# Kernel optimization log

Measured on AMD Instinct MI355X. Metric: run time of the kernel, lower is better.

Reference implementation:

```python
import jax, jax.numpy as jnp
import numpy as np

B, F, Q, CHUNK = 2, 8192, 4096, 512
NUM_VERTS = 6000


def _safe_div(n, d):
    return n / jnp.where(d == 0, 1.0, d)


def _bary(a, b, c, p):
    """Barycentric coords of the closest point on triangle (a,b,c) to p.
    All args broadcastable [..., 3]; returns [..., 3] (u, v, w) with
    closest = u*a + v*b + w*c. Ericson, Real-Time Collision Detection."""
    ab = b - a; ac = c - a; ap = p - a
    d1 = jnp.sum(ab * ap, -1); d2 = jnp.sum(ac * ap, -1)
    bp = p - b
    d3 = jnp.sum(ab * bp, -1); d4 = jnp.sum(ac * bp, -1)
    cp_ = p - c
    d5 = jnp.sum(ab * cp_, -1); d6 = jnp.sum(ac * cp_, -1)
    vc = d1 * d4 - d3 * d2
    vb = d5 * d2 - d1 * d6
    va = d3 * d6 - d5 * d4
    v_ab = _safe_div(d1, d1 - d3)
    w_ac = _safe_div(d2, d2 - d6)
    w_bc = _safe_div(d4 - d3, (d4 - d3) + (d5 - d6))
    inv = _safe_div(1.0, va + vb + vc)
    v_in = vb * inv; w_in = vc * inv
    zero = jnp.zeros_like(d1); one = jnp.ones_like(d1)
    conds = [(d1 <= 0) & (d2 <= 0),
             (d3 >= 0) & (d4 <= d3),
             (vc <= 0) & (d1 >= 0) & (d3 <= 0),
             (d6 >= 0) & (d5 <= d6),
             (vb <= 0) & (d2 >= 0) & (d6 <= 0),
             (va <= 0) & (d4 >= d3) & (d5 >= d6)]
    u = jnp.select(conds, [one, zero, 1 - v_ab, zero, 1 - w_ac, zero], 1 - v_in - w_in)
    v = jnp.select(conds, [zero, one, v_ab, zero, zero, 1 - w_bc], v_in)
    w = jnp.select(conds, [zero, zero, zero, one, w_ac, w_bc], w_in)
    return jnp.stack([u, v, w], -1)


def _closest_faces(triangles, points, chunk=CHUNK):
    """Exact closest-triangle index per query point (replaces BVH search).
    triangles [B,F,3,3], points [B,Q,3] -> int32 [B,Q]."""
    tri = jax.lax.stop_gradient(triangles)
    pts = jax.lax.stop_gradient(points)
    bsz, nq = pts.shape[0], pts.shape[1]
    a = tri[:, :, 0]; b = tri[:, :, 1]; c = tri[:, :, 2]  # [B,F,3]

    def one_chunk(p_chunk):  # [B,CH,3]
        pa = p_chunk[:, :, None, :]                       # [B,CH,1,3]
        bc = _bary(a[:, None], b[:, None], c[:, None], pa)  # [B,CH,F,3]
        cp = (bc[..., 0:1] * a[:, None] + bc[..., 1:2] * b[:, None]
              + bc[..., 2:3] * c[:, None])                # [B,CH,F,3]
        d2 = jnp.sum((cp - pa) ** 2, -1)                  # [B,CH,F]
        return jnp.argmin(d2, axis=-1)                    # [B,CH]

    chunks = jnp.moveaxis(pts.reshape(bsz, nq // chunk, chunk, 3), 1, 0)
    idx = jax.lax.map(one_chunk, chunks)                  # [NC,B,CH]
    return jnp.moveaxis(idx, 0, 1).reshape(bsz, nq)


def setup_inputs() -> dict:
    key = jax.random.key(0)
    k1, k2, k3, k4, k5 = jax.random.split(key, 5)
    return {
        'triangles': jax.random.normal(k1, (B, F, 3, 3), dtype=jnp.float32),
        'points': jax.random.normal(k2, (B, Q, 3), dtype=jnp.float32),
        'normals': jax.random.normal(k3, (B, F, 3, 3), dtype=jnp.float32),
        'cmaps': jax.random.normal(k4, (B, F, 3, 3), dtype=jnp.float32),
        'faces': jax.random.randint(k5, (B, F, 3), 0, NUM_VERTS, dtype=jnp.int32),
    }


def reference(triangles, points, normals, cmaps, faces):
    closest_faces = _closest_faces(triangles, points)     # [B,Q]
    idx = closest_faces[:, :, None, None]
    tri_g = jnp.take_along_axis(triangles, idx, axis=1)   # [B,Q,3,3]
    nrm_g = jnp.take_along_axis(normals, idx, axis=1)
    cmp_g = jnp.take_along_axis(cmaps, idx, axis=1)
    bcs = _bary(tri_g[:, :, 0], tri_g[:, :, 1], tri_g[:, :, 2], points)  # [B,Q,3]
    bcs = jnp.clip(bcs, 0.0, 1.0)
    closest_points = jnp.einsum('bqk,bqkd->bqd', bcs, tri_g)
    closest_normals = jnp.einsum('bqk,bqkd->bqd', bcs, nrm_g)
    closest_cmaps = jnp.einsum('bqk,bqkd->bqd', bcs, cmp_g)
    residual = closest_points - points
    closest_fids = jnp.take_along_axis(faces, closest_faces[:, :, None], axis=1)  # [B,Q,3]
    closest_idx = jnp.take_along_axis(
        closest_fids, jnp.argmax(bcs, -1)[:, :, None], axis=2)[..., 0]            # [B,Q]
    return residual, closest_normals, closest_cmaps, closest_idx
```

## Files before the change

### kernel.cpp

```cpp
#include <hip/hip_runtime.h>
#include <float.h>

#define B_   2
#define F_   8192
#define Q_   4096
#define NC   64
#define FC   (F_/NC)
#define PTS  256
#define PPT  2

typedef float f2 __attribute__((ext_vector_type(2)));

__device__ __forceinline__ f2 clamp01(f2 x) {
    f2 z = {0.f, 0.f}, o = {1.f, 1.f};
    return __builtin_elementwise_min(__builtin_elementwise_max(x, z), o);
}

__device__ __forceinline__ void bary_uvw(
    float ax, float ay, float az,
    float bx, float by, float bz,
    float cx, float cy, float cz,
    float px, float py, float pz,
    float& u, float& v, float& w)
{
#pragma clang fp contract(off)
    float abx = bx - ax, aby = by - ay, abz = bz - az;
    float acx = cx - ax, acy = cy - ay, acz = cz - az;
    float apx = px - ax, apy = py - ay, apz = pz - az;
    float d1 = abx*apx + aby*apy + abz*apz;
    float d2 = acx*apx + acy*apy + acz*apz;
    float bpx = px - bx, bpy = py - by, bpz = pz - bz;
    float d3 = abx*bpx + aby*bpy + abz*bpz;
    float d4 = acx*bpx + acy*bpy + acz*bpz;
    float qx = px - cx, qy = py - cy, qz = pz - cz;
    float d5 = abx*qx + aby*qy + abz*qz;
    float d6 = acx*qx + acy*qy + acz*qz;
    float vc = d1*d4 - d3*d2;
    float vb = d5*d2 - d1*d6;
    float va = d3*d6 - d5*d4;

    bool c1 = (d1 <= 0.f) && (d2 <= 0.f);
    bool c2 = (d3 >= 0.f) && (d4 <= d3);
    bool c3 = (vc <= 0.f) && (d1 >= 0.f) && (d3 <= 0.f);
    bool c4 = (d6 >= 0.f) && (d5 <= d6);
    bool c5 = (vb <= 0.f) && (d2 >= 0.f) && (d6 <= 0.f);
    bool c6 = (va <= 0.f) && (d4 >= d3) && (d5 >= d6);

    bool e1 = c1;
    bool p1 = !c1;
    bool e2 = p1 && c2;
    bool p2 = p1 && !c2;
    bool e3 = p2 && c3;
    bool p3 = p2 && !c3;
    bool e4 = p3 && c4;
    bool p4 = p3 && !c4;
    bool e5 = p4 && c5;
    bool p5 = p4 && !c5;
    bool e6 = p5 && c6;

    float d43 = d4 - d3;
    float d56 = d5 - d6;
    float n  = e3 ? d1        : (e5 ? d2        : (e6 ? d43         : 1.f));
    float dd = e3 ? (d1 - d3) : (e5 ? (d2 - d6) : (e6 ? (d43 + d56) : (va + vb + vc)));
    dd = (dd == 0.f) ? 1.f : dd;
    float t = n / dd;

    float vi = vb * t;
    float wi = vc * t;
    u = e1 ? 1.f : (e2 ? 0.f : (e3 ? 1.f - t : (e4 ? 0.f : (e5 ? 1.f - t : (e6 ? 0.f     : 1.f - vi - wi)))));
    v = e1 ? 0.f : (e2 ? 1.f : (e3 ? t       : (e4 ? 0.f : (e5 ? 0.f     : (e6 ? 1.f - t : vi)))));
    w = e1 ? 0.f : (e2 ? 0.f : (e3 ? 0.f     : (e4 ? 1.f : (e5 ? t       : (e6 ? t       : wi)))));
}

__global__ __launch_bounds__(PTS) void scan_kernel(
    const float* __restrict__ tri, const float* __restrict__ pts,
    int* __restrict__ pix)
{
    __shared__ float4 S[FC * 4];
    const int tid = threadIdx.x;
    const int pb = blockIdx.x, cb = blockIdx.y, bb = blockIdx.z;

    {
        const int tr = tid & (FC - 1);
        const int hf = tid >> 7;
        const float* g = tri + ((size_t)bb * F_ + (size_t)cb * FC + tr) * 9;
        float ax = g[0], ay = g[1], az = g[2];
        float bx = g[3], by = g[4], bz = g[5];
        float cx = g[6], cy = g[7], cz = g[8];
        float abx = bx - ax, aby = by - ay, abz = bz - az;
        float acx = cx - ax, acy = cy - ay, acz = cz - az;
        float daa = abx*abx + aby*aby + abz*abz;
        float dcc = acx*acx + acy*acy + acz*acz;
        float dac = abx*acx + aby*acy + abz*acz;
        float dbc = daa + dcc - 2.f*dac;
        float nn  = daa*dcc - dac*dac;
        if (hf == 0) {
            S[tr*4 + 0] = make_float4(ax, ay, az, daa);
            S[tr*4 + 1] = make_float4(abx, aby, abz, dcc);
        } else {
            S[tr*4 + 2] = make_float4(acx, acy, acz, dac);
            S[tr*4 + 3] = make_float4(1.f/daa, 1.f/dcc, 1.f/dbc, 1.f/nn);
        }
    }
    __syncthreads();

    const int q0 = pb * (PTS * PPT) + tid * PPT;
    const float* p0 = pts + ((size_t)bb * Q_ + q0) * 3;
    f2 px = {p0[0], p0[3]};
    f2 py = {p0[1], p0[4]};
    f2 pz = {p0[2], p0[5]};

    float bA0 = FLT_MAX, bA1 = FLT_MAX;
    float bB0 = FLT_MAX, bB1 = FLT_MAX;
    int iA0 = 0, iA1 = 0, iB0 = 0, iB1 = 0;
    #pragma unroll 2
    for (int fl = 0; fl < FC; ++fl) {
        float4 c0 = S[fl*4 + 0];
        float4 c1 = S[fl*4 + 1];
        float4 c2 = S[fl*4 + 2];
        float4 c3 = S[fl*4 + 3];
        float daa = c0.w, dcc = c1.w, dac = c2.w;
        float dbc = daa + dcc - 2.f*dac;

        f2 apx = px - c0.x, apy = py - c0.y, apz = pz - c0.z;
        f2 d1  = c1.x*apx + c1.y*apy + c1.z*apz;
        f2 d2  = c2.x*apx + c2.y*apy + c2.z*apz;
        f2 app = apx*apx + apy*apy + apz*apz;
        f2 d3 = d1 - daa, d4 = d2 - dac, d5 = d1 - dac, d6 = d2 - dcc;
        f2 d43 = d4 - d3;
        f2 va = d3*d6 - d5*d4;
        f2 vb = d5*d2 - d1*d6;
        f2 vc = d1*d4 - d3*d2;

        f2 t1 = d1*dcc - d2*dac;
        f2 t2 = d2*daa - d1*dac;
        f2 sg = d1*t1 + d2*t2;
        f2 dint = app - sg*c3.w;

        f2 td1 = d1 + d1;
        f2 tab = clamp01(d1 * c3.x);
        f2 eab = app - tab*(td1 - tab*daa);
        f2 tac = clamp01(d2 * c3.y);
        f2 eac = app - tac*(d2 + d2 - tac*dcc);
        f2 bpp = app - td1 + daa;
        f2 sbc = clamp01(d43 * c3.z);
        f2 ebc = bpp - sbc*(d43 + d43 - sbc*dbc);

        f2 emin = __builtin_elementwise_min(__builtin_elementwise_min(eab, eac), ebc);

        bool in0 = (va.x >= 0.f) && (vb.x >= 0.f) && (vc.x >= 0.f);
        bool in1 = (va.y >= 0.f) && (vb.y >= 0.f) && (vc.y >= 0.f);
        float dA = in0 ? dint.x : emin.x;
        float dB = in1 ? dint.y : emin.y;

        bool a1 = dA < bA0, a2 = dA < bA1;
        bA1 = a1 ? bA0 : (a2 ? dA : bA1);
        iA1 = a1 ? iA0 : (a2 ? fl : iA1);
        bA0 = a1 ? dA : bA0;
        iA0 = a1 ? fl : iA0;
        bool b1 = dB < bB0, b2 = dB < bB1;
        bB1 = b1 ? bB0 : (b2 ? dB : bB1);
        iB1 = b1 ? iB0 : (b2 ? fl : iB1);
        bB0 = b1 ? dB : bB0;
        iB0 = b1 ? fl : iB0;
    }

    const int fb = cb * FC;
    size_t o = ((size_t)bb * Q_ + q0) * NC + cb;
    pix[o]      = (fb + iA0) | ((fb + iA1) << 16);
    pix[o + NC] = (fb + iB0) | ((fb + iB1) << 16);
}

__global__ __launch_bounds__(256) void finalize_kernel(
    const float* __restrict__ tri, const float* __restrict__ pts,
    const float* __restrict__ nrm, const float* __restrict__ cmp,
    const int* __restrict__ faces,
    const int* __restrict__ pix,
    float* __restrict__ out)
{
#pragma clang fp contract(off)
    const int lane = threadIdx.x & 63;
    const int t = blockIdx.x * 4 + (threadIdx.x >> 6);
    const int bb = t / Q_;

    const float* pp = pts + (size_t)t * 3;
    float px = pp[0], py = pp[1], pz = pp[2];

    int pk = pix[(size_t)t * NC + lane];
    int fc0 = pk & 0xFFFF;
    int fc1 = (pk >> 16) & 0xFFFF;

    float dbest; int fbest;
    {
        float dcand[2]; int fcand[2] = {fc0, fc1};
        #pragma unroll
        for (int j = 0; j < 2; ++j) {
            const float* tg = tri + ((size_t)bb * F_ + fcand[j]) * 9;
            float ax = tg[0], ay = tg[1], az = tg[2];
            float bx = tg[3], by = tg[4], bz = tg[5];
            float cx = tg[6], cy = tg[7], cz = tg[8];
            float u, v, w;
            bary_uvw(ax, ay, az, bx, by, bz, cx, cy, cz, px, py, pz, u, v, w);
            float cpx = u*ax + v*bx + w*cx;
            float cpy = u*ay + v*by + w*cy;
            float cpz = u*az + v*bz + w*cz;
            float dx = cpx - px, dy = cpy - py, dz = cpz - pz;
            dcand[j] = dx*dx + dy*dy + dz*dz;
        }
        if (dcand[1] < dcand[0] || (dcand[1] == dcand[0] && fcand[1] < fcand[0])) {
            dbest = dcand[1]; fbest = fcand[1];
        } else {
            dbest = dcand[0]; fbest = fcand[0];
        }
        for (int off = 32; off > 0; off >>= 1) {
            float od = __shfl_down(dbest, off);
            int   of = __shfl_down(fbest, off);
            if (od < dbest || (od == dbest && of < fbest)) { dbest = od; fbest = of; }
        }
        fbest = __shfl(fbest, 0);
    }
    if (lane != 0) return;

    const int bestf = fbest;
    const float* tg = tri + ((size_t)bb * F_ + bestf) * 9;
    const float* ng = nrm + ((size_t)bb * F_ + bestf) * 9;
    const float* cg = cmp + ((size_t)bb * F_ + bestf) * 9;

    float u, v, w;
    bary_uvw(tg[0], tg[1], tg[2],  tg[3], tg[4], tg[5],  tg[6], tg[7], tg[8],
             px, py, pz, u, v, w);
    u = fminf(fmaxf(u, 0.f), 1.f);
    v = fminf(fmaxf(v, 0.f), 1.f);
    w = fminf(fmaxf(w, 0.f), 1.f);

    float cpx = u * tg[0] + v * tg[3] + w * tg[6];
    float cpy = u * tg[1] + v * tg[4] + w * tg[7];
    float cpz = u * tg[2] + v * tg[5] + w * tg[8];
    float nx  = u * ng[0] + v * ng[3] + w * ng[6];
    float ny  = u * ng[1] + v * ng[4] + w * ng[7];
    float nz  = u * ng[2] + v * ng[5] + w * ng[8];
    float mx  = u * cg[0] + v * cg[3] + w * cg[6];
    float my  = u * cg[1] + v * cg[4] + w * cg[7];
    float mz  = u * cg[2] + v * cg[5] + w * cg[8];

    const size_t S3 = (size_t)B_ * Q_ * 3;
    out[(size_t)t * 3 + 0] = cpx - px;
    out[(size_t)t * 3 + 1] = cpy - py;
    out[(size_t)t * 3 + 2] = cpz - pz;
    out[S3 + (size_t)t * 3 + 0] = nx;
    out[S3 + (size_t)t * 3 + 1] = ny;
    out[S3 + (size_t)t * 3 + 2] = nz;
    out[2 * S3 + (size_t)t * 3 + 0] = mx;
    out[2 * S3 + (size_t)t * 3 + 1] = my;
    out[2 * S3 + (size_t)t * 3 + 2] = mz;

    int k = 0; float m = u;
    if (v > m) { m = v; k = 1; }
    if (w > m) { k = 2; }
    out[3 * S3 + t] = (float)faces[((size_t)bb * F_ + bestf) * 3 + k];
}

extern "C" void kernel_launch(void* const* d_in, const int* in_sizes, int n_in,
                              void* d_out, int out_size, void* d_ws, size_t ws_size,
                              hipStream_t stream) {
    const float* tri   = (const float*)d_in[0];
    const float* pts   = (const float*)d_in[1];
    const float* nrm   = (const float*)d_in[2];
    const float* cmp   = (const float*)d_in[3];
    const int*   faces = (const int*)d_in[4];
    float* out = (float*)d_out;

    int* pix = (int*)d_ws;

    dim3 g1(Q_ / (PTS * PPT), NC, B_);
    scan_kernel<<<g1, PTS, 0, stream>>>(tri, pts, pix);
    finalize_kernel<<<(B_ * Q_) / 4, 256, 0, stream>>>(
        tri, pts, nrm, cmp, faces, pix, out);
}
```

Baseline: 152.6 us.

## Pack distance and index into sortable keys, simplify inside test, double face chunks

The scan kernel now keeps its top-2 candidates as packed 32-bit keys. Each key is a clamped, non-negative float distance with its low 6 bits replaced by the local face index, so selection needs only integer min/max instead of compare-and-select chains. The inside-triangle test reuses the barycentric numerators t1/t2 already computed, replacing the va/vb/vc products. NC doubles to 128 so each block scans 64 faces, with 8 blocks per SM requested through launch bounds. The finalize kernel then re-evaluates four candidates per lane exactly. Truncating the distance mantissa can mis-rank near-ties, which the exact finalize pass is meant to absorb. The cost is double the workspace traffic and more finalize work.

```diff
diff --git a/kernel.cpp b/kernel.cpp
--- a/kernel.cpp
+++ b/kernel.cpp
@@ -4,12 +4,13 @@
 #define B_   2
 #define F_   8192
 #define Q_   4096
-#define NC   64
+#define NC   128
 #define FC   (F_/NC)
 #define PTS  256
 #define PPT  2
 
 typedef float f2 __attribute__((ext_vector_type(2)));
+typedef unsigned int uint;
 
 __device__ __forceinline__ f2 clamp01(f2 x) {
     f2 z = {0.f, 0.f}, o = {1.f, 1.f};
@@ -72,9 +73,9 @@
     w = e1 ? 0.f : (e2 ? 0.f : (e3 ? 0.f     : (e4 ? 1.f : (e5 ? t       : (e6 ? t       : wi)))));
 }
 
-__global__ __launch_bounds__(PTS) void scan_kernel(
+__global__ __launch_bounds__(PTS, 8) void scan_kernel(
     const float* __restrict__ tri, const float* __restrict__ pts,
-    int* __restrict__ pix)
+    uint2* __restrict__ keys)
 {
     __shared__ float4 S[FC * 4];
     const int tid = threadIdx.x;
@@ -82,7 +83,7 @@
 
     {
         const int tr = tid & (FC - 1);
-        const int hf = tid >> 7;
+        const int qt = tid >> 6;
         const float* g = tri + ((size_t)bb * F_ + (size_t)cb * FC + tr) * 9;
         float ax = g[0], ay = g[1], az = g[2];
         float bx = g[3], by = g[4], bz = g[5];
@@ -92,15 +93,16 @@
         float daa = abx*abx + aby*aby + abz*abz;
         float dcc = acx*acx + acy*acy + acz*acz;
         float dac = abx*acx + aby*acy + abz*acz;
-        float dbc = daa + dcc - 2.f*dac;
-        float nn  = daa*dcc - dac*dac;
-        if (hf == 0) {
-            S[tr*4 + 0] = make_float4(ax, ay, az, daa);
-            S[tr*4 + 1] = make_float4(abx, aby, abz, dcc);
-        } else {
-            S[tr*4 + 2] = make_float4(acx, acy, acz, dac);
-            S[tr*4 + 3] = make_float4(1.f/daa, 1.f/dcc, 1.f/dbc, 1.f/nn);
+        float4 v;
+        if (qt == 0)      v = make_float4(ax, ay, az, daa);
+        else if (qt == 1) v = make_float4(abx, aby, abz, dcc);
+        else if (qt == 2) v = make_float4(acx, acy, acz, dac);
+        else {
+            float dbc = daa + dcc - 2.f*dac;
+            float nn  = daa*dcc - dac*dac;
+            v = make_float4(1.f/daa, 1.f/dcc, 1.f/dbc, 1.f/nn);
         }
+        S[tr*4 + qt] = v;
     }
     __syncthreads();
 
@@ -110,9 +112,8 @@
     f2 py = {p0[1], p0[4]};
     f2 pz = {p0[2], p0[5]};
 
-    float bA0 = FLT_MAX, bA1 = FLT_MAX;
-    float bB0 = FLT_MAX, bB1 = FLT_MAX;
-    int iA0 = 0, iA1 = 0, iB0 = 0, iB1 = 0;
+    uint a0 = 0xFFFFFFFFu, a1 = 0xFFFFFFFFu;
+    uint b0 = 0xFFFFFFFFu, b1 = 0xFFFFFFFFu;
     #pragma unroll 2
     for (int fl = 0; fl < FC; ++fl) {
         float4 c0 = S[fl*4 + 0];
@@ -121,61 +122,53 @@
         float4 c3 = S[fl*4 + 3];
         float daa = c0.w, dcc = c1.w, dac = c2.w;
         float dbc = daa + dcc - 2.f*dac;
+        float nn  = daa*dcc - dac*dac;
+        float kk  = daa - dac;
 
         f2 apx = px - c0.x, apy = py - c0.y, apz = pz - c0.z;
         f2 d1  = c1.x*apx + c1.y*apy + c1.z*apz;
         f2 d2  = c2.x*apx + c2.y*apy + c2.z*apz;
         f2 app = apx*apx + apy*apy + apz*apz;
-        f2 d3 = d1 - daa, d4 = d2 - dac, d5 = d1 - dac, d6 = d2 - dcc;
-        f2 d43 = d4 - d3;
-        f2 va = d3*d6 - d5*d4;
-        f2 vb = d5*d2 - d1*d6;
-        f2 vc = d1*d4 - d3*d2;
-
-        f2 t1 = d1*dcc - d2*dac;
-        f2 t2 = d2*daa - d1*dac;
-        f2 sg = d1*t1 + d2*t2;
+        f2 t1  = d1*dcc - d2*dac;
+        f2 t2  = d2*daa - d1*dac;
+        f2 t12 = t1 + t2;
+        f2 sg  = d1*t1 + d2*t2;
         f2 dint = app - sg*c3.w;
 
+        f2 d43 = (d2 - d1) + kk;
         f2 td1 = d1 + d1;
         f2 tab = clamp01(d1 * c3.x);
         f2 eab = app - tab*(td1 - tab*daa);
         f2 tac = clamp01(d2 * c3.y);
-        f2 eac = app - tac*(d2 + d2 - tac*dcc);
-        f2 bpp = app - td1 + daa;
+        f2 eac = app - tac*((d2 + d2) - tac*dcc);
+        f2 bpp = (app - td1) + daa;
         f2 sbc = clamp01(d43 * c3.z);
-        f2 ebc = bpp - sbc*(d43 + d43 - sbc*dbc);
-
+        f2 ebc = bpp - sbc*((d43 + d43) - sbc*dbc);
         f2 emin = __builtin_elementwise_min(__builtin_elementwise_min(eab, eac), ebc);
 
-        bool in0 = (va.x >= 0.f) && (vb.x >= 0.f) && (vc.x >= 0.f);
-        bool in1 = (va.y >= 0.f) && (vb.y >= 0.f) && (vc.y >= 0.f);
-        float dA = in0 ? dint.x : emin.x;
-        float dB = in1 ? dint.y : emin.y;
-
-        bool a1 = dA < bA0, a2 = dA < bA1;
-        bA1 = a1 ? bA0 : (a2 ? dA : bA1);
-        iA1 = a1 ? iA0 : (a2 ? fl : iA1);
-        bA0 = a1 ? dA : bA0;
-        iA0 = a1 ? fl : iA0;
-        bool b1 = dB < bB0, b2 = dB < bB1;
-        bB1 = b1 ? bB0 : (b2 ? dB : bB1);
-        iB1 = b1 ? iB0 : (b2 ? fl : iB1);
-        bB0 = b1 ? dB : bB0;
-        iB0 = b1 ? fl : iB0;
-    }
-
-    const int fb = cb * FC;
+        bool inA = (t1.x >= 0.f) & (t2.x >= 0.f) & (t12.x <= nn);
+        bool inB = (t1.y >= 0.f) & (t2.y >= 0.f) & (t12.y <= nn);
+        float dA = fmaxf(inA ? dint.x : emin.x, 0.f);
+        float dB = fmaxf(inB ? dint.y : emin.y, 0.f);
+
+        uint kA = (__float_as_uint(dA) & 0xFFFFFFC0u) | (uint)fl;
+        uint kB = (__float_as_uint(dB) & 0xFFFFFFC0u) | (uint)fl;
+        uint lo = min(a0, kA), hi = max(a0, kA);
+        a0 = lo; a1 = min(a1, hi);
+        lo = min(b0, kB); hi = max(b0, kB);
+        b0 = lo; b1 = min(b1, hi);
+    }
+
     size_t o = ((size_t)bb * Q_ + q0) * NC + cb;
-    pix[o]      = (fb + iA0) | ((fb + iA1) << 16);
-    pix[o + NC] = (fb + iB0) | ((fb + iB1) << 16);
+    keys[o]      = make_uint2(a0, a1);
+    keys[o + NC] = make_uint2(b0, b1);
 }
 
 __global__ __launch_bounds__(256) void finalize_kernel(
     const float* __restrict__ tri, const float* __restrict__ pts,
     const float* __restrict__ nrm, const float* __restrict__ cmp,
     const int* __restrict__ faces,
-    const int* __restrict__ pix,
+    const uint* __restrict__ keys,
     float* __restrict__ out)
 {
 #pragma clang fp contract(off)
@@ -186,39 +179,33 @@
     const float* pp = pts + (size_t)t * 3;
     float px = pp[0], py = pp[1], pz = pp[2];
 
-    int pk = pix[(size_t)t * NC + lane];
-    int fc0 = pk & 0xFFFF;
-    int fc1 = (pk >> 16) & 0xFFFF;
-
-    float dbest; int fbest;
-    {
-        float dcand[2]; int fcand[2] = {fc0, fc1};
-        #pragma unroll
-        for (int j = 0; j < 2; ++j) {
-            const float* tg = tri + ((size_t)bb * F_ + fcand[j]) * 9;
-            float ax = tg[0], ay = tg[1], az = tg[2];
-            float bx = tg[3], by = tg[4], bz = tg[5];
-            float cx = tg[6], cy = tg[7], cz = tg[8];
-            float u, v, w;
-            bary_uvw(ax, ay, az, bx, by, bz, cx, cy, cz, px, py, pz, u, v, w);
-            float cpx = u*ax + v*bx + w*cx;
-            float cpy = u*ay + v*by + w*cy;
-            float cpz = u*az + v*bz + w*cz;
-            float dx = cpx - px, dy = cpy - py, dz = cpz - pz;
-            dcand[j] = dx*dx + dy*dy + dz*dz;
-        }
-        if (dcand[1] < dcand[0] || (dcand[1] == dcand[0] && fcand[1] < fcand[0])) {
-            dbest = dcand[1]; fbest = fcand[1];
-        } else {
-            dbest = dcand[0]; fbest = fcand[0];
-        }
-        for (int off = 32; off > 0; off >>= 1) {
-            float od = __shfl_down(dbest, off);
-            int   of = __shfl_down(fbest, off);
-            if (od < dbest || (od == dbest && of < fbest)) { dbest = od; fbest = of; }
-        }
-        fbest = __shfl(fbest, 0);
-    }
+    const uint4* kp = (const uint4*)keys;
+    uint4 K = kp[(size_t)t * (NC/2) + lane];
+
+    float dbest = FLT_MAX; int fbest = 0x7FFFFFFF;
+    uint kj[4] = {K.x, K.y, K.z, K.w};
+    #pragma unroll
+    for (int j = 0; j < 4; ++j) {
+        int face = (2*lane + (j >> 1)) * FC + (int)(kj[j] & 63u);
+        const float* tg = tri + ((size_t)bb * F_ + face) * 9;
+        float ax = tg[0], ay = tg[1], az = tg[2];
+        float bx = tg[3], by = tg[4], bz = tg[5];
+        float cx = tg[6], cy = tg[7], cz = tg[8];
+        float u, v, w;
+        bary_uvw(ax, ay, az, bx, by, bz, cx, cy, cz, px, py, pz, u, v, w);
+        float cpx = u*ax + v*bx + w*cx;
+        float cpy = u*ay + v*by + w*cy;
+        float cpz = u*az + v*bz + w*cz;
+        float dx = cpx - px, dy = cpy - py, dz = cpz - pz;
+        float d2v = dx*dx + dy*dy + dz*dz;
+        if (d2v < dbest || (d2v == dbest && face < fbest)) { dbest = d2v; fbest = face; }
+    }
+    for (int off = 32; off > 0; off >>= 1) {
+        float od = __shfl_down(dbest, off);
+        int   of = __shfl_down(fbest, off);
+        if (od < dbest || (od == dbest && of < fbest)) { dbest = od; fbest = of; }
+    }
+    fbest = __shfl(fbest, 0);
     if (lane != 0) return;
 
     const int bestf = fbest;
@@ -254,9 +241,9 @@
     out[2 * S3 + (size_t)t * 3 + 1] = my;
     out[2 * S3 + (size_t)t * 3 + 2] = mz;
 
-    int k = 0; float m = u;
-    if (v > m) { m = v; k = 1; }
-    if (w > m) { k = 2; }
+    int k = 0; float mm = u;
+    if (v > mm) { mm = v; k = 1; }
+    if (w > mm) { k = 2; }
     out[3 * S3 + t] = (float)faces[((size_t)bb * F_ + bestf) * 3 + k];
 }
 
@@ -270,10 +257,10 @@
     const int*   faces = (const int*)d_in[4];
     float* out = (float*)d_out;
 
-    int* pix = (int*)d_ws;
+    uint2* keys = (uint2*)d_ws;
 
     dim3 g1(Q_ / (PTS * PPT), NC, B_);
-    scan_kernel<<<g1, PTS, 0, stream>>>(tri, pts, pix);
+    scan_kernel<<<g1, PTS, 0, stream>>>(tri, pts, keys);
     finalize_kernel<<<(B_ * Q_) / 4, 256, 0, stream>>>(
-        tri, pts, nrm, cmp, faces, pix, out);
-}
+        tri, pts, nrm, cmp, faces, (const uint*)keys, out);
+}
```

After: 155.2 us. About the same (+1.7%).
